# Performance work log

Measured on AMD Instinct MI355X. Metric: run time of the kernel, lower is better.

Reference implementation:

```python
import jax, jax.numpy as jnp
import numpy as np
import math

SAMPLE_RATIO = 0.25
K = 5
EPS = 1e-6

def _cells(loc_orig, H, W):
    # map normalized [-1,1] coords to nearest grid cell index, as in tcformer token2map/map2token
    loc = jnp.clip(loc_orig, -1.0, 1.0)
    px = jnp.clip(jnp.round(0.5 * (loc[..., 0] + 1.0) * W - 0.5).astype(jnp.int32), 0, W - 1)
    py = jnp.clip(jnp.round(0.5 * (loc[..., 1] + 1.0) * H - 0.5).astype(jnp.int32), 0, H - 1)
    return py * W + px  # [B, N0]

def token2map(x, loc_orig, idx_agg, H, W):
    B, N, C = x.shape
    N0 = loc_orig.shape[1]
    cell = _cells(loc_orig, H, W)
    seg = (cell + jnp.arange(B)[:, None] * (H * W)).reshape(-1)
    feat = x[jnp.arange(B)[:, None], idx_agg]  # [B, N0, C] token feature per original point
    sums = jax.ops.segment_sum(feat.reshape(-1, C), seg, num_segments=B * H * W)
    cnt = jax.ops.segment_sum(jnp.ones((B * N0,), x.dtype), seg, num_segments=B * H * W)
    x_map = sums / (cnt[:, None] + EPS)  # per-cell mean over points hitting the cell
    return x_map.reshape(B, H, W, C).transpose(0, 3, 1, 2)

def map2token(x_map, N, loc_orig, idx_agg, agg_weight):
    B, C, H, W = x_map.shape
    cell = _cells(loc_orig, H, W)
    val = x_map.reshape(B, C, H * W).transpose(0, 2, 1)  # [B, HW, C]
    vpt = val[jnp.arange(B)[:, None], cell]              # [B, N0, C] map value at each point
    seg = (idx_agg + jnp.arange(B)[:, None] * N).reshape(-1)
    w = agg_weight.reshape(-1)
    wsum = jax.ops.segment_sum(w, seg, num_segments=B * N) + EPS
    ssum = jax.ops.segment_sum(vpt.reshape(-1, C) * w[:, None], seg, num_segments=B * N)
    return (ssum / wsum[:, None]).reshape(B, N, C)  # agg_weight-weighted mean per token

def token_cluster_merge(x, Ns, idx_agg, weight, k):
    B, N, C = x.shape
    # DPC-KNN clustering (index computation; mirrors torch.no_grad block)
    sq = jnp.sum(x * x, -1)
    d2 = jnp.clip(sq[:, :, None] + sq[:, None, :] - 2.0 * jnp.einsum('bnc,bmc->bnm', x, x), 0.0, None)
    dist = jnp.sqrt(d2) / (C ** 0.5)
    dnear = -jax.lax.top_k(-dist, k)[0]                  # k smallest distances (incl. self)
    density = jnp.exp(-jnp.mean(dnear * dnear, -1))
    mask = density[:, None, :] > density[:, :, None]
    dmax = jnp.max(dist.reshape(B, -1), -1)[:, None, None]
    parent_dist = jnp.min(jnp.where(mask, dist, dmax), -1)  # dist to nearest higher-density token
    score = parent_dist * density
    index_down = jax.lax.top_k(score, Ns)[1]             # [B, Ns] cluster centers
    idx_cluster = jnp.argmin(dist[jnp.arange(B)[:, None], index_down], axis=1)  # [B, N]
    idx_cluster = idx_cluster.at[jnp.arange(B)[:, None], index_down].set(jnp.arange(Ns)[None, :])
    # weighted merge of tokens into clusters
    seg = (idx_cluster + jnp.arange(B)[:, None] * Ns).reshape(-1)
    w = weight.reshape(-1)
    allw = jax.ops.segment_sum(w, seg, num_segments=B * Ns) + EPS
    norm_w = (w / allw[seg]).reshape(B, N)
    x_merged = jax.ops.segment_sum((x * norm_w[:, :, None]).reshape(-1, C), seg, num_segments=B * Ns).reshape(B, Ns, C)
    idx_agg_down = idx_cluster[jnp.arange(B)[:, None], idx_agg]      # compose index maps
    weight_t = norm_w[jnp.arange(B)[:, None], idx_agg][..., None]    # [B, N0, 1]
    return x_merged, idx_agg_down, weight_t

def _forward(x, loc_orig, idx_agg, agg_weight, idx_k_loc, H, W, conv_w, conv_b, skip_w, ln_g, ln_b, conf_w, conf_b):
    B, N, C = x.shape
    x_map = token2map(x, loc_orig, idx_agg, H, W)
    x_map = jax.lax.conv_general_dilated(x_map, conv_w, (2, 2), ((1, 1), (1, 1))) + conv_b[None, :, None, None]
    x_tok = map2token(x_map, N, loc_orig, idx_agg, agg_weight) + jnp.einsum('bnc,oc->bno', x, skip_w)
    mu = jnp.mean(x_tok, -1, keepdims=True)
    var = jnp.mean((x_tok - mu) ** 2, -1, keepdims=True)
    x_tok = (x_tok - mu) / jnp.sqrt(var + 1e-5) * ln_g + ln_b
    conf = jnp.einsum('bnc,oc->bno', x_tok, conf_w) + conf_b
    weight = jnp.exp(conf)
    Ns = max(math.ceil(N * SAMPLE_RATIO), 1)
    x_down, idx_agg_down, weight_t = token_cluster_merge(x_tok, Ns, idx_agg, weight, K)
    agg_weight_down = agg_weight * weight_t
    agg_weight_down = agg_weight_down / jnp.max(agg_weight_down, axis=1, keepdims=True)
    # down_block is an injected submodule; treated as identity passthrough here
    return x_down, idx_agg_down, agg_weight_down

def setup_inputs():
    key = jax.random.key(0)
    ks = jax.random.split(key, 8)
    B, N, C, N0, Cout = 8, 256, 256, 16384, 512
    return {
        'x': jax.random.normal(ks[0], (B, N, C), jnp.float32),
        'loc_orig': jax.random.uniform(ks[1], (B, N0, 2), jnp.float32, -1.0, 1.0),
        'idx_agg': jax.random.randint(ks[2], (B, N0), 0, N),
        'agg_weight': jax.random.uniform(ks[3], (B, N0, 1), jnp.float32, 0.1, 1.0),
        'idx_k_loc': jax.random.randint(ks[4], (B, N0, K), 0, N0),
        'H': 64, 'W': 64,
        'conv_w': jax.random.normal(ks[5], (Cout, C, 3, 3), jnp.float32) * 0.02,
        'conv_b': jnp.zeros((Cout,), jnp.float32),
        'skip_w': jax.random.normal(ks[6], (Cout, C), jnp.float32) * 0.02,
        'ln_g': jnp.ones((Cout,), jnp.float32),
        'ln_b': jnp.zeros((Cout,), jnp.float32),
        'conf_w': jax.random.normal(ks[7], (1, Cout), jnp.float32) * 0.02,
        'conf_b': jnp.zeros((1,), jnp.float32),
    }

def reference(x, loc_orig, idx_agg, agg_weight, idx_k_loc, H, W, conv_w, conv_b, skip_w, ln_g, ln_b, conf_w, conf_b):
    return _forward(x, loc_orig, idx_agg, agg_weight, idx_k_loc, H, W, conv_w, conv_b, skip_w, ln_g, ln_b, conf_w, conf_b)
```

## Files before the change

kernel.cpp:

```cpp
#include <hip/hip_runtime.h>
#include <math.h>

typedef unsigned long long ull;
typedef __attribute__((ext_vector_type(8))) short short8v;
typedef __attribute__((ext_vector_type(4))) float float4v;

#define NB   8
#define NTOK 256
#define CIN  256
#define NP   16384
#define NCO  512
#define HW64 4096
#define OHW  1024
#define NS   64
#define EPS  1e-6f
#define KC   2304
#define NKC  72

constexpr size_t OFF_SUMS = 0;
constexpr size_t OFF_CNT  = OFF_SUMS + (size_t)NB*HW64*CIN;
constexpr size_t OFF_AMAT = OFF_CNT  + (size_t)NB*HW64;
constexpr size_t OFF_ALLW = OFF_AMAT + (size_t)NB*NTOK*OHW;
constexpr size_t OFF_DMAX = OFF_ALLW + (size_t)NB*NS;
constexpr size_t OFF_MAXW = OFF_DMAX + NB;
constexpr size_t ZERO_END = OFF_MAXW + NB;
constexpr size_t OFF_WT   = ZERO_END;
constexpr size_t OFF_SKWT = OFF_WT   + (size_t)KC*NCO;
constexpr size_t OFF_Y    = OFF_SKWT + (size_t)CIN*NCO;
constexpr size_t OFF_C2   = OFF_Y    + (size_t)NB*OHW*NCO;
constexpr size_t OFF_WSUM = OFF_C2   + (size_t)NB*NTOK*NCO;
constexpr size_t OFF_XSKIP= OFF_WSUM + (size_t)NB*NTOK;
constexpr size_t OFF_XTOK = OFF_XSKIP+ (size_t)NB*NTOK*NCO;
constexpr size_t OFF_XPK  = OFF_XTOK + (size_t)NB*NTOK*NCO;
constexpr size_t OFF_WEXP = OFF_XPK  + (size_t)NB*NTOK*NCO;
constexpr size_t OFF_SQ   = OFF_WEXP + (size_t)NB*NTOK;
constexpr size_t OFF_DIST = OFF_SQ   + (size_t)NB*NTOK;
constexpr size_t OFF_DENS = OFF_DIST + (size_t)NB*NTOK*NTOK;
constexpr size_t OFF_SCORE= OFF_DENS + (size_t)NB*NTOK;
constexpr size_t OFF_IND  = OFF_SCORE+ (size_t)NB*NTOK;
constexpr size_t OFF_IDXCL= OFF_IND  + (size_t)NB*NS;
constexpr size_t OFF_NORMW= OFF_IDXCL+ (size_t)NB*NTOK;
constexpr size_t OFF_AWBUF= OFF_NORMW+ (size_t)NB*NTOK;
constexpr size_t OFF_XTPK = OFF_AWBUF+ (size_t)NB*NP;
constexpr size_t OFF_AMATP = OFF_SUMS;
constexpr size_t OFF_XTOKPK= OFF_Y;

__device__ __forceinline__ unsigned pack_hl(float x) {
    unsigned u = __float_as_uint(x);
    unsigned t = u + 0x7fffu + ((u >> 16) & 1u);
    unsigned hibits = t & 0xffff0000u;
    float lo = x - __uint_as_float(hibits);
    unsigned ul = __float_as_uint(lo);
    unsigned lt = ul + 0x7fffu + ((ul >> 16) & 1u);
    return hibits | (lt >> 16);
}
__device__ __forceinline__ unsigned hp2(unsigned w0, unsigned w1) {
    return __builtin_amdgcn_perm(w1, w0, 0x07060302u);
}
__device__ __forceinline__ unsigned lp2(unsigned w0, unsigned w1) {
    return __builtin_amdgcn_perm(w1, w0, 0x05040100u);
}

__global__ void hist(const float* __restrict__ loc, const int* __restrict__ idxagg,
                     const float* __restrict__ aggw,
                     int* __restrict__ cntmat, float* __restrict__ cnt,
                     float* __restrict__ amat) {
    int bp = blockIdx.x*256 + threadIdx.x;
    int b  = bp >> 14;
    float lx = loc[2*bp+0], ly = loc[2*bp+1];
    lx = fminf(fmaxf(lx, -1.f), 1.f);
    ly = fminf(fmaxf(ly, -1.f), 1.f);
    int px = (int)rintf((lx + 1.f)*32.f - 0.5f); px = min(max(px,0),63);
    int py = (int)rintf((ly + 1.f)*32.f - 0.5f); py = min(max(py,0),63);
    int cell = py*64 + px;
    int tok = idxagg[bp];
    atomicAdd(&cntmat[((size_t)(b*HW64 + cell))*NTOK + tok], 1);
    atomicAdd(&cnt[b*HW64 + cell], 1.0f);
    int qx = (int)rintf((lx + 1.f)*16.f - 0.5f); qx = min(max(qx,0),31);
    int qy = (int)rintf((ly + 1.f)*16.f - 0.5f); qy = min(max(qy,0),31);
    atomicAdd(&amat[((size_t)(b*NTOK + tok))*OHW + qy*32 + qx], aggw[bp]);
}

__global__ void cnt_pack(unsigned* __restrict__ m) {
    size_t i = (size_t)blockIdx.x*256 + threadIdx.x;
    int4 v = ((const int4*)m)[i];
    uint4 o;
    o.x = pack_hl((float)v.x); o.y = pack_hl((float)v.y);
    o.z = pack_hl((float)v.z); o.w = pack_hl((float)v.w);
    ((uint4*)m)[i] = o;
}

__global__ void xt_pack(const float* __restrict__ x, unsigned* __restrict__ xtpk) {
    int id = blockIdx.x*256 + threadIdx.x;
    int tok = id & 255, cin = (id >> 8) & 255, b = id >> 16;
    xtpk[id] = pack_hl(x[((size_t)(b*NTOK + tok))*CIN + cin]);
}

__global__ void wtrans(const float* __restrict__ convw, uint4* __restrict__ wtf) {
    int tid = blockIdx.x*256 + threadIdx.x;
    int lane = tid & 63;
    int r1 = tid >> 6;
    int h = r1 & 1;
    int r2 = r1 >> 1;
    int f = r2 & 3;
    int r3 = r2 >> 2;
    int kc = r3 % NKC, mt = r3 / NKC;
    int cout = mt*64 + f*16 + (lane & 15);
    int kb = kc*32 + (lane >> 4)*8;
    unsigned s[8];
    #pragma unroll
    for (int j = 0; j < 8; ++j) {
        int k = kb + j;
        int grp = k >> 8, cin = k & 255;
        unsigned w = pack_hl(convw[(size_t)cout*KC + cin*9 + grp]);
        s[j] = h ? (w & 0xffffu) : (w >> 16);
    }
    uint4 o;
    o.x = s[0] | (s[1]<<16); o.y = s[2] | (s[3]<<16);
    o.z = s[4] | (s[5]<<16); o.w = s[6] | (s[7]<<16);
    wtf[tid] = o;
}

__global__ void pack4(const float4* __restrict__ src, uint4* __restrict__ dst) {
    size_t i = (size_t)blockIdx.x*256 + threadIdx.x;
    float4 v = src[i];
    uint4 o;
    o.x = pack_hl(v.x); o.y = pack_hl(v.y); o.z = pack_hl(v.z); o.w = pack_hl(v.w);
    dst[i] = o;
}

__launch_bounds__(256)
__global__ void conv_gemm(const unsigned* __restrict__ xmap, const uint4* __restrict__ wtf,
                          const float* __restrict__ convb, unsigned* __restrict__ ytp) {
    __shared__ __align__(16) unsigned short Ahi[2][4096], Alo[2][4096];
    int n0 = blockIdx.x * 128;
    int mt = blockIdx.y;
    int m0 = mt * 64;
    int t = threadIdx.x;
    int lane = t & 63, wid = t >> 6;
    int wm = wid >> 1, wn = wid & 1;
    int l15 = lane & 15, l4 = lane >> 4;

    int rowL = t & 127, kg = t >> 7;
    int posG = n0 + rowL;
    int bb = posG >> 10, rem = posG & 1023;
    int oy = rem >> 5, ox = rem & 31;

    int wbA0 = (rowL>>4)*512 + kg*128 + (rowL&15)*8;
    int wbA1 = wbA0 + 256;

    float4v acc[4][2] = {};
    uint4 a00,a01,a10,a11;

    auto loadA = [&](int kc) {
        int grp = kc >> 3;
        int ky = grp/3, kx = grp - 3*ky;
        int iy = 2*oy - 1 + ky, ix = 2*ox - 1 + kx;
        if ((unsigned)iy < 64u && (unsigned)ix < 64u) {
            const unsigned* ap = xmap + ((((size_t)bb*64 + iy)*64 + ix)*256 + (kc&7)*32 + kg*8);
            a00 = *(const uint4*)ap;       a01 = *(const uint4*)(ap + 4);
            a10 = *(const uint4*)(ap + 16); a11 = *(const uint4*)(ap + 20);
        } else {
            a00 = make_uint4(0,0,0,0); a01 = a00; a10 = a00; a11 = a00;
        }
    };
    auto repackA = [&](int buf) {
        uint4 h, l;
        h.x=hp2(a00.x,a00.y); h.y=hp2(a00.z,a00.w); h.z=hp2(a01.x,a01.y); h.w=hp2(a01.z,a01.w);
        l.x=lp2(a00.x,a00.y); l.y=lp2(a00.z,a00.w); l.z=lp2(a01.x,a01.y); l.w=lp2(a01.z,a01.w);
        *(uint4*)&Ahi[buf][wbA0] = h; *(uint4*)&Alo[buf][wbA0] = l;
        h.x=hp2(a10.x,a10.y); h.y=hp2(a10.z,a10.w); h.z=hp2(a11.x,a11.y); h.w=hp2(a11.z,a11.w);
        l.x=lp2(a10.x,a10.y); l.y=lp2(a10.z,a10.w); l.z=lp2(a11.x,a11.y); l.w=lp2(a11.z,a11.w);
        *(uint4*)&Ahi[buf][wbA1] = h; *(uint4*)&Alo[buf][wbA1] = l;
    };
    const uint4* wbase = wtf + ((size_t)(((mt*NKC)*4 + wn*2)*2))*64 + lane;

    short8v bhc[2], blc[2], bhn[2], bln[2];
    #pragma unroll
    for (int q = 0; q < 2; ++q) {
        bhc[q] = *(const short8v*)(wbase + q*128);
        blc[q] = *(const short8v*)(wbase + q*128 + 64);
    }
    loadA(0);
    repackA(0);
    __syncthreads();
    int cur = 0;

    for (int kc = 0; kc < NKC; ++kc) {
        bool notlast = (kc + 1 < NKC);
        if (notlast) {
            loadA(kc+1);
            const uint4* wb = wbase + (size_t)(kc+1)*512;
            #pragma unroll
            for (int q = 0; q < 2; ++q) {
                bhn[q] = *(const short8v*)(wb + q*128);
                bln[q] = *(const short8v*)(wb + q*128 + 64);
            }
        }
        #pragma unroll
        for (int p = 0; p < 4; ++p) {
            int off = (wm*4 + p)*512 + l4*128 + l15*8;
            short8v ah = *(const short8v*)&Ahi[cur][off];
            short8v al = *(const short8v*)&Alo[cur][off];
            #pragma unroll
            for (int q = 0; q < 2; ++q) {
                acc[p][q] = __builtin_amdgcn_mfma_f32_16x16x32_bf16(ah, bhc[q], acc[p][q], 0, 0, 0);
                acc[p][q] = __builtin_amdgcn_mfma_f32_16x16x32_bf16(ah, blc[q], acc[p][q], 0, 0, 0);
                acc[p][q] = __builtin_amdgcn_mfma_f32_16x16x32_bf16(al, bhc[q], acc[p][q], 0, 0, 0);
            }
        }
        if (notlast) {
            repackA(cur ^ 1);
            #pragma unroll
            for (int q = 0; q < 2; ++q) { bhc[q] = bhn[q]; blc[q] = bln[q]; }
        }
        __syncthreads();
        cur ^= 1;
    }

    int bbk = n0 >> 10;
    int pos0 = (n0 & 1023) + wm*64;
    #pragma unroll
    for (int p = 0; p < 4; ++p) {
        int posb = pos0 + p*16 + l4*4;
        #pragma unroll
        for (int q = 0; q < 2; ++q) {
            int col = m0 + wn*32 + q*16 + l15;
            float bv = convb[col];
            uint4 o;
            o.x = pack_hl(acc[p][q][0] + bv);
            o.y = pack_hl(acc[p][q][1] + bv);
            o.z = pack_hl(acc[p][q][2] + bv);
            o.w = pack_hl(acc[p][q][3] + bv);
            *(uint4*)&ytp[((size_t)(bbk*NCO + col))*OHW + posb] = o;
        }
    }
}

template<int MODE, int TM, int TN>
__launch_bounds__(256)
__global__ void gemm_pk(const unsigned* __restrict__ A, const unsigned* __restrict__ B,
                        float* __restrict__ C, int K, int N,
                        long sA, long sB, long sC,
                        const float* __restrict__ aux, unsigned* __restrict__ dmaxU) {
    constexpr int NA = TM/64, NBs = TN/64;
    constexpr int WSM = TM/64;
    constexpr int WSN = 4/WSM;
    constexpr int TWM = TM/WSM, TWN = TN/WSN;
    constexpr int P = TWM/16, Q = TWN/16;
    __shared__ __align__(16) unsigned short Ahi[TM*32], Alo[TM*32];
    __shared__ __align__(16) unsigned short Bhi[TN*32], Blo[TN*32];
    int z = blockIdx.z;
    const unsigned* Ab = A + (size_t)z*sA;
    const unsigned* Bb = B + (size_t)z*sB;
    float* Cb = C + (size_t)z*sC;
    int n0 = blockIdx.x*TN, m0 = blockIdx.y*TM;
    int t = threadIdx.x;
    int lane = t & 63, wid = t >> 6;
    int wm = (WSM==2) ? (wid >> 1) : 0;
    int wn = (WSM==2) ? (wid & 1)  : wid;
    int l15 = lane & 15, l4 = lane >> 4;

    int rowA = t & (TM-1), kgA = t / TM;
    int rowB = t & (TN-1), kgB = t / TN;
    const unsigned* arow = Ab + (size_t)(m0 + rowA)*K + kgA*8;
    const unsigned* brw  = Bb + (size_t)(n0 + rowB)*K + kgB*8;
    int wbA = (rowA>>4)*512 + kgA*128 + (rowA&15)*8;
    int wbB = (rowB>>4)*512 + kgB*128 + (rowB&15)*8;

    float4v acc[P][Q] = {};
    uint4 ra[NA][2], rb[NBs][2];
    auto loadA = [&](int kc) {
        #pragma unroll
        for (int s = 0; s < NA; ++s) {
            const unsigned* p = arow + (size_t)kc*32 + s*16;
            ra[s][0] = *(const uint4*)p; ra[s][1] = *(const uint4*)(p + 4);
        }
    };
    auto loadB = [&](int kc) {
        #pragma unroll
        for (int s = 0; s < NBs; ++s) {
            const unsigned* p = brw + (size_t)kc*32 + s*16;
            rb[s][0] = *(const uint4*)p; rb[s][1] = *(const uint4*)(p + 4);
        }
    };
    loadA(0); loadB(0);
    int nkc = K >> 5;

    for (int kc = 0; kc < nkc; ++kc) {
        __syncthreads();
        uint4 h, l;
        #pragma unroll
        for (int s = 0; s < NA; ++s) {
            uint4 u0 = ra[s][0], u1 = ra[s][1];
            h.x=hp2(u0.x,u0.y); h.y=hp2(u0.z,u0.w); h.z=hp2(u1.x,u1.y); h.w=hp2(u1.z,u1.w);
            l.x=lp2(u0.x,u0.y); l.y=lp2(u0.z,u0.w); l.z=lp2(u1.x,u1.y); l.w=lp2(u1.z,u1.w);
            *(uint4*)&Ahi[wbA + s*256] = h; *(uint4*)&Alo[wbA + s*256] = l;
        }
        #pragma unroll
        for (int s = 0; s < NBs; ++s) {
            uint4 u0 = rb[s][0], u1 = rb[s][1];
            h.x=hp2(u0.x,u0.y); h.y=hp2(u0.z,u0.w); h.z=hp2(u1.x,u1.y); h.w=hp2(u1.z,u1.w);
            l.x=lp2(u0.x,u0.y); l.y=lp2(u0.z,u0.w); l.z=lp2(u1.x,u1.y); l.w=lp2(u1.z,u1.w);
            *(uint4*)&Bhi[wbB + s*256] = h; *(uint4*)&Blo[wbB + s*256] = l;
        }
        __syncthreads();
        if (kc + 1 < nkc) { loadA(kc+1); loadB(kc+1); }

        short8v bh[Q], bl[Q];
        #pragma unroll
        for (int q = 0; q < Q; ++q) {
            int off = (wn*Q + q)*512 + l4*128 + l15*8;
            bh[q] = *(const short8v*)&Bhi[off];
            bl[q] = *(const short8v*)&Blo[off];
        }
        #pragma unroll
        for (int p = 0; p < P; ++p) {
            int off = (wm*P + p)*512 + l4*128 + l15*8;
            short8v ah = *(const short8v*)&Ahi[off];
            short8v al = *(const short8v*)&Alo[off];
            #pragma unroll
            for (int q = 0; q < Q; ++q) {
                acc[p][q] = __builtin_amdgcn_mfma_f32_16x16x32_bf16(ah, bh[q], acc[p][q], 0, 0, 0);
                acc[p][q] = __builtin_amdgcn_mfma_f32_16x16x32_bf16(ah, bl[q], acc[p][q], 0, 0, 0);
                acc[p][q] = __builtin_amdgcn_mfma_f32_16x16x32_bf16(al, bh[q], acc[p][q], 0, 0, 0);
            }
        }
    }

    if (MODE == 0) {
        #pragma unroll
        for (int p = 0; p < P; ++p) {
            int mb = m0 + wm*TWM + p*16 + l4*4;
            #pragma unroll
            for (int q = 0; q < Q; ++q) {
                int n = n0 + wn*TWN + q*16 + l15;
                #pragma unroll
                for (int r = 0; r < 4; ++r)
                    Cb[(size_t)(mb + r)*N + n] = acc[p][q][r];
            }
        }
    } else if (MODE == 1) {
        const float inv = 1.0f / sqrtf(512.0f);
        const float* sqb = aux + (size_t)z*NTOK;
        float tmax = 0.f;
        #pragma unroll
        for (int p = 0; p < P; ++p) {
            int mb = m0 + wm*TWM + p*16 + l4*4;
            #pragma unroll
            for (int q = 0; q < Q; ++q) {
                int n = n0 + wn*TWN + q*16 + l15;
                float sn = sqb[n];
                #pragma unroll
                for (int r = 0; r < 4; ++r) {
                    float d2 = sqb[mb + r] + sn - 2.0f*acc[p][q][r];
                    float d = sqrtf(fmaxf(d2, 0.0f)) * inv;
                    Cb[(size_t)(mb + r)*N + n] = d;
                    tmax = fmaxf(tmax, d);
                }
            }
        }
        __shared__ float redm[4];
        #pragma unroll
        for (int off = 32; off; off >>= 1) tmax = fmaxf(tmax, __shfl_xor(tmax, off, 64));
        if (lane == 0) redm[wid] = tmax;
        __syncthreads();
        if (t == 0) {
            float m = fmaxf(fmaxf(redm[0], redm[1]), fmaxf(redm[2], redm[3]));
            atomicMax(dmaxU + z, __float_as_uint(m));
        }
    } else {
        unsigned* Cu = (unsigned*)Cb;
        const float* cntb = aux + (size_t)z*HW64;
        #pragma unroll
        for (int p = 0; p < P; ++p) {
            int mb = m0 + wm*TWM + p*16 + l4*4;
            #pragma unroll
            for (int q = 0; q < Q; ++q) {
                int n = n0 + wn*TWN + q*16 + l15;
                #pragma unroll
                for (int r = 0; r < 4; ++r) {
                    float v = acc[p][q][r] / (cntb[mb + r] + EPS);
                    Cu[(size_t)(mb + r)*N + n] = pack_hl(v);
                }
            }
        }
    }
}

__global__ void wsum_rows(const float* __restrict__ amat, float* __restrict__ wsum) {
    int row = blockIdx.x*4 + (threadIdx.x >> 6);
    int lane = threadIdx.x & 63;
    const float* ar = amat + (size_t)row*OHW;
    float s = 0.f;
    #pragma unroll
    for (int r = 0; r < 16; ++r) s += ar[lane + 64*r];
    #pragma unroll
    for (int off = 32; off; off >>= 1) s += __shfl_xor(s, off, 64);
    if (lane == 0) wsum[row] = s;
}

__device__ __forceinline__ float block_sum256(float v, float* red) {
    #pragma unroll
    for (int off = 32; off; off >>= 1) v += __shfl_xor(v, off, 64);
    __syncthreads();
    if ((threadIdx.x & 63) == 0) red[threadIdx.x >> 6] = v;
    __syncthreads();
    return red[0] + red[1] + red[2] + red[3];
}

__global__ void ln_conf(const float* __restrict__ C2, const float* __restrict__ wsum,
                        const float* __restrict__ xskip, const float* __restrict__ g,
                        const float* __restrict__ be, const float* __restrict__ confw,
                        const float* __restrict__ confb, float* __restrict__ xtok,
                        unsigned* __restrict__ xtokpk,
                        float* __restrict__ wexp, float* __restrict__ sqv) {
    __shared__ float red[4];
    int row = blockIdx.x, t = threadIdx.x;
    float ws = wsum[row] + EPS;
    size_t base = (size_t)row*NCO;
    float v0 = C2[base + t]       / ws + xskip[base + t];
    float v1 = C2[base + t + 256] / ws + xskip[base + t + 256];
    float mu  = block_sum256(v0 + v1, red) / 512.0f;
    float d0 = v0 - mu, d1 = v1 - mu;
    float var = block_sum256(d0*d0 + d1*d1, red) / 512.0f;
    float sv = sqrtf(var + 1e-5f);
    float x0 = d0/sv * g[t]       + be[t];
    float x1 = d1/sv * g[t + 256] + be[t + 256];
    xtok[base + t] = x0;
    xtok[base + t + 256] = x1;
    xtokpk[base + t] = pack_hl(x0);
    xtokpk[base + t + 256] = pack_hl(x1);
    float cs = block_sum256(x0*confw[t] + x1*confw[t + 256], red);
    float qs = block_sum256(x0*x0 + x1*x1, red);
    if (t == 0) {
        wexp[row] = expf(cs + confb[0]);
        sqv[row]  = qs;
    }
}

__global__ void knn_dens(const float* __restrict__ dist, float* __restrict__ dens) {
    int row = blockIdx.x*4 + (threadIdx.x >> 6);
    int lane = threadIdx.x & 63;
    const float* dr = dist + (size_t)row*NTOK;
    float v0 = dr[lane], v1 = dr[lane+64], v2 = dr[lane+128], v3 = dr[lane+192];
    float acc = 0.f;
    #pragma unroll
    for (int it = 0; it < 5; ++it) {
        float lm = fminf(fminf(v0, v1), fminf(v2, v3));
        float gm = lm;
        #pragma unroll
        for (int off = 32; off; off >>= 1) gm = fminf(gm, __shfl_xor(gm, off, 64));
        acc += gm*gm;
        ull ball = __ballot(lm == gm);
        int first = __ffsll(ball) - 1;
        if (lane == first) {
            if      (v0 == gm) v0 = 1e30f;
            else if (v1 == gm) v1 = 1e30f;
            else if (v2 == gm) v2 = 1e30f;
            else               v3 = 1e30f;
        }
    }
    if (lane == 0) dens[row] = expf(-(acc/5.0f));
}

__global__ void parent_score(const float* __restrict__ dist, const float* __restrict__ dens,
                             const unsigned* __restrict__ dmaxU, float* __restrict__ score) {
    int row = blockIdx.x*4 + (threadIdx.x >> 6);
    int lane = threadIdx.x & 63;
    int b = row >> 8;
    float di = dens[row];
    float dm = __uint_as_float(dmaxU[b]);
    const float* dr = dist + (size_t)row*NTOK;
    const float* db = dens + (size_t)b*NTOK;
    float pd = dm;
    #pragma unroll
    for (int r = 0; r < 4; ++r) {
        int j = lane + 64*r;
        pd = fminf(pd, (db[j] > di) ? dr[j] : dm);
    }
    #pragma unroll
    for (int off = 32; off; off >>= 1) pd = fminf(pd, __shfl_xor(pd, off, 64));
    if (lane == 0) score[row] = pd * di;
}

__global__ void topk64(const float* __restrict__ score, int* __restrict__ ind) {
    int b = blockIdx.x, lane = threadIdx.x;
    const float* sb = score + b*NTOK;
    ull k0, k1, k2, k3;
    {
        unsigned i0 = lane, i1 = lane+64, i2 = lane+128, i3 = lane+192;
        k0 = ((ull)(__float_as_uint(sb[i0]) + 1u) << 32) | (unsigned)(4095 - i0);
        k1 = ((ull)(__float_as_uint(sb[i1]) + 1u) << 32) | (unsigned)(4095 - i1);
        k2 = ((ull)(__float_as_uint(sb[i2]) + 1u) << 32) | (unsigned)(4095 - i2);
        k3 = ((ull)(__float_as_uint(sb[i3]) + 1u) << 32) | (unsigned)(4095 - i3);
    }
    for (int it = 0; it < 64; ++it) {
        ull lm = k0;
        if (k1 > lm) lm = k1;
        if (k2 > lm) lm = k2;
        if (k3 > lm) lm = k3;
        ull gm = lm;
        #pragma unroll
        for (int off = 32; off; off >>= 1) {
            ull o = __shfl_xor(gm, off, 64);
            if (o > gm) gm = o;
        }
        if (lane == 0) ind[b*NS + it] = 4095 - (int)(gm & 0xffffffffull);
        if      (k0 == gm) k0 = 0;
        else if (k1 == gm) k1 = 0;
        else if (k2 == gm) k2 = 0;
        else if (k3 == gm) k3 = 0;
    }
}

__global__ void assign_k(const float* __restrict__ dist, const int* __restrict__ ind,
                         int* __restrict__ idxcl) {
    int row = blockIdx.x*4 + (threadIdx.x >> 6);
    int lane = threadIdx.x & 63;
    int b = row >> 8, i = row & 255;
    int center = ind[b*NS + lane];
    float d = dist[((size_t)(b*NTOK + center))*NTOK + i];
    ull key = ((ull)__float_as_uint(d) << 32) | (unsigned)lane;
    #pragma unroll
    for (int off = 32; off; off >>= 1) {
        ull o = __shfl_xor(key, off, 64);
        if (o < key) key = o;
    }
    if (lane == 0) idxcl[row] = (int)(key & 0xffffffffull);
}

__global__ void center_set(const int* __restrict__ ind, int* __restrict__ idxcl) {
    int id = threadIdx.x;
    int b = id >> 6, s = id & 63;
    idxcl[b*NTOK + ind[id]] = s;
}

__global__ void allw_acc(const int* __restrict__ idxcl, const float* __restrict__ wexp,
                         float* __restrict__ allw) {
    int b = blockIdx.x, i = threadIdx.x;
    atomicAdd(&allw[b*NS + idxcl[b*NTOK + i]], wexp[b*NTOK + i]);
}

__global__ void normw_k(const int* __restrict__ idxcl, const float* __restrict__ wexp,
                        const float* __restrict__ allw, float* __restrict__ normw) {
    int b = blockIdx.x, i = threadIdx.x;
    normw[b*NTOK + i] = wexp[b*NTOK + i] / (allw[b*NS + idxcl[b*NTOK + i]] + EPS);
}

__global__ void merge_k(const float* __restrict__ xtok, const int* __restrict__ idxcl,
                        const float* __restrict__ normw, float* __restrict__ xout) {
    int row = blockIdx.x, t = threadIdx.x;
    int b = row >> 8;
    int cl = idxcl[row];
    float nw = normw[row];
    float* o = xout + ((size_t)(b*NS + cl))*NCO;
    const float* xr = xtok + (size_t)row*NCO;
    atomicAdd(&o[t],       xr[t]       * nw);
    atomicAdd(&o[t + 256], xr[t + 256] * nw);
}

__global__ void out_idx_aw(const int* __restrict__ idxagg, const float* __restrict__ aggw,
                           const int* __restrict__ idxcl, const float* __restrict__ normw,
                           float* __restrict__ dout, float* __restrict__ awbuf,
                           unsigned* __restrict__ maxw) {
    __shared__ float red[4];
    int bp = blockIdx.x*256 + threadIdx.x;
    int b = bp >> 14;
    int tok = idxagg[bp];
    int cl = idxcl[b*NTOK + tok];
    dout[(size_t)NB*NS*NCO + bp] = (float)cl;
    float aw = aggw[bp] * normw[b*NTOK + tok];
    awbuf[bp] = aw;
    float m = aw;
    #pragma unroll
    for (int off = 32; off; off >>= 1) m = fmaxf(m, __shfl_xor(m, off, 64));
    if ((threadIdx.x & 63) == 0) red[threadIdx.x >> 6] = m;
    __syncthreads();
    if (threadIdx.x == 0) {
        float mm = fmaxf(fmaxf(red[0], red[1]), fmaxf(red[2], red[3]));
        atomicMax(&maxw[b], __float_as_uint(mm));
    }
}

__global__ void aw_final(const float* __restrict__ awbuf, const float* __restrict__ maxw,
                         float* __restrict__ dout) {
    int bp = blockIdx.x*256 + threadIdx.x;
    int b = bp >> 14;
    dout[(size_t)NB*NS*NCO + (size_t)NB*NP + bp] = awbuf[bp] / maxw[b];
}

extern "C" void kernel_launch(void* const* d_in, const int* in_sizes, int n_in,
                              void* d_out, int out_size, void* d_ws, size_t ws_size,
                              hipStream_t stream) {
    const float* x      = (const float*)d_in[0];
    const float* loc    = (const float*)d_in[1];
    const int*   idxagg = (const int*)  d_in[2];
    const float* aggw   = (const float*)d_in[3];
    const float* convw  = (const float*)d_in[7];
    const float* convb  = (const float*)d_in[8];
    const float* skipw  = (const float*)d_in[9];
    const float* lng    = (const float*)d_in[10];
    const float* lnb    = (const float*)d_in[11];
    const float* confw  = (const float*)d_in[12];
    const float* confb  = (const float*)d_in[13];

    float* ws = (float*)d_ws;
    float* dout = (float*)d_out;

    (void)hipMemsetAsync(ws, 0, ZERO_END*sizeof(float), stream);
    (void)hipMemsetAsync(dout, 0, (size_t)NB*NS*NCO*sizeof(float), stream);

    hist<<<dim3(NB*NP/256), 256, 0, stream>>>(loc, idxagg, aggw,
                                              (int*)(ws + OFF_SUMS), ws + OFF_CNT, ws + OFF_AMAT);
    cnt_pack<<<dim3(NB*HW64*CIN/1024), 256, 0, stream>>>((unsigned*)(ws + OFF_SUMS));
    xt_pack<<<dim3(NB*CIN*NTOK/256), 256, 0, stream>>>(x, (unsigned*)(ws + OFF_XTPK));
    wtrans<<<dim3(1152), 256, 0, stream>>>(convw, (uint4*)(ws + OFF_WT));
    pack4<<<dim3(CIN*NCO/1024), 256, 0, stream>>>((const float4*)skipw, (uint4*)(ws + OFF_SKWT));
    pack4<<<dim3(NB*NTOK*CIN/1024), 256, 0, stream>>>((const float4*)x, (uint4*)(ws + OFF_XPK));

    gemm_pk<2,128,128><<<dim3(2, 32, 8), 256, 0, stream>>>((const unsigned*)(ws + OFF_SUMS),
                                                   (const unsigned*)(ws + OFF_XTPK),
                                                   ws + OFF_SUMS, NTOK, CIN,
                                                   (long)HW64*NTOK, (long)CIN*NTOK, (long)HW64*CIN,
                                                   ws + OFF_CNT, nullptr);

    conv_gemm<<<dim3(64, 8), 256, 0, stream>>>((const unsigned*)(ws + OFF_SUMS),
                                               (const uint4*)(ws + OFF_WT), convb,
                                               (unsigned*)(ws + OFF_Y));

    wsum_rows<<<dim3(NB*NTOK/4), 256, 0, stream>>>(ws + OFF_AMAT, ws + OFF_WSUM);
    pack4<<<dim3(NB*NTOK*OHW/1024), 256, 0, stream>>>((const float4*)(ws + OFF_AMAT),
                                                      (uint4*)(ws + OFF_AMATP));
    gemm_pk<0,64,64><<<dim3(8, 4, 8), 256, 0, stream>>>((const unsigned*)(ws + OFF_AMATP),
                                                  (const unsigned*)(ws + OFF_Y),
                                                  ws + OFF_C2, OHW, NCO,
                                                  (long)NTOK*OHW, (long)NCO*OHW, (long)NTOK*NCO,
                                                  nullptr, nullptr);
    gemm_pk<0,64,64><<<dim3(8, 32, 1), 256, 0, stream>>>((const unsigned*)(ws + OFF_XPK),
                                                   (const unsigned*)(ws + OFF_SKWT),
                                                   ws + OFF_XSKIP, CIN, NCO, 0, 0, 0,
                                                   nullptr, nullptr);

    ln_conf<<<dim3(NB*NTOK), 256, 0, stream>>>(ws + OFF_C2, ws + OFF_WSUM, ws + OFF_XSKIP,
                                               lng, lnb, confw, confb,
                                               ws + OFF_XTOK, (unsigned*)(ws + OFF_XTOKPK),
                                               ws + OFF_WEXP, ws + OFF_SQ);

    gemm_pk<1,64,64><<<dim3(4, 4, 8), 256, 0, stream>>>((const unsigned*)(ws + OFF_XTOKPK),
                                                  (const unsigned*)(ws + OFF_XTOKPK),
                                                  ws + OFF_DIST, NCO, NTOK,
                                                  (long)NTOK*NCO, (long)NTOK*NCO, (long)NTOK*NTOK,
                                                  ws + OFF_SQ, (unsigned*)(ws + OFF_DMAX));

    knn_dens<<<dim3(NB*NTOK/4), 256, 0, stream>>>(ws + OFF_DIST, ws + OFF_DENS);
    parent_score<<<dim3(NB*NTOK/4), 256, 0, stream>>>(ws + OFF_DIST, ws + OFF_DENS,
                                                      (const unsigned*)(ws + OFF_DMAX), ws + OFF_SCORE);
    topk64<<<dim3(NB), 64, 0, stream>>>(ws + OFF_SCORE, (int*)(ws + OFF_IND));
    assign_k<<<dim3(NB*NTOK/4), 256, 0, stream>>>(ws + OFF_DIST, (const int*)(ws + OFF_IND),
                                                  (int*)(ws + OFF_IDXCL));
    center_set<<<dim3(1), 512, 0, stream>>>((const int*)(ws + OFF_IND), (int*)(ws + OFF_IDXCL));
    allw_acc<<<dim3(NB), 256, 0, stream>>>((const int*)(ws + OFF_IDXCL), ws + OFF_WEXP, ws + OFF_ALLW);
    normw_k<<<dim3(NB), 256, 0, stream>>>((const int*)(ws + OFF_IDXCL), ws + OFF_WEXP,
                                          ws + OFF_ALLW, ws + OFF_NORMW);
    merge_k<<<dim3(NB*NTOK), 256, 0, stream>>>(ws + OFF_XTOK, (const int*)(ws + OFF_IDXCL),
                                               ws + OFF_NORMW, dout);
    out_idx_aw<<<dim3(NB*NP/256), 256, 0, stream>>>(idxagg, aggw, (const int*)(ws + OFF_IDXCL),
                                                    ws + OFF_NORMW, dout, ws + OFF_AWBUF,
                                                    (unsigned*)(ws + OFF_MAXW));
    aw_final<<<dim3(NB*NP/256), 256, 0, stream>>>(ws + OFF_AWBUF, (const float*)(ws + OFF_MAXW), dout);
}
```

Before: 304.3 us.

## Store token map as split bf16 hi/lo planes and stage conv A via global_load_lds

The token-to-map GEMM now lives in its own kernel. It writes the normalized map as separate hi and lo bf16 planes in a 128-row tiled layout, replacing packed hi/lo words. The conv GEMM then copies A tiles straight from global into LDS with global_load_lds. Out-of-bounds taps point at a zeroed guard buffer, which removes the register staging and permute repack in the main loop. The packed amat buffer moves to a new offset so it no longer aliases the planes, at the cost of strided 16-bit stores in the map epilogue.

```diff
diff --git a/kernel.cpp b/kernel.cpp
--- a/kernel.cpp
+++ b/kernel.cpp
@@ -17,13 +17,20 @@
 #define KC   2304
 #define NKC  72
 
+#define AS1 __attribute__((address_space(1)))
+#define AS3 __attribute__((address_space(3)))
+__device__ __forceinline__ void gl_lds16(const unsigned short* g, unsigned short* l) {
+    __builtin_amdgcn_global_load_lds((const AS1 unsigned*)g, (AS3 unsigned*)l, 16, 0, 0);
+}
+
 constexpr size_t OFF_SUMS = 0;
 constexpr size_t OFF_CNT  = OFF_SUMS + (size_t)NB*HW64*CIN;
 constexpr size_t OFF_AMAT = OFF_CNT  + (size_t)NB*HW64;
 constexpr size_t OFF_ALLW = OFF_AMAT + (size_t)NB*NTOK*OHW;
 constexpr size_t OFF_DMAX = OFF_ALLW + (size_t)NB*NS;
 constexpr size_t OFF_MAXW = OFF_DMAX + NB;
-constexpr size_t ZERO_END = OFF_MAXW + NB;
+constexpr size_t OFF_ZG   = OFF_MAXW + NB;
+constexpr size_t ZERO_END = OFF_ZG + 8;
 constexpr size_t OFF_WT   = ZERO_END;
 constexpr size_t OFF_SKWT = OFF_WT   + (size_t)KC*NCO;
 constexpr size_t OFF_Y    = OFF_SKWT + (size_t)CIN*NCO;
@@ -42,7 +49,7 @@
 constexpr size_t OFF_NORMW= OFF_IDXCL+ (size_t)NB*NTOK;
 constexpr size_t OFF_AWBUF= OFF_NORMW+ (size_t)NB*NTOK;
 constexpr size_t OFF_XTPK = OFF_AWBUF+ (size_t)NB*NP;
-constexpr size_t OFF_AMATP = OFF_SUMS;
+constexpr size_t OFF_AMATP2= OFF_XTPK + (size_t)NB*CIN*NTOK;
 constexpr size_t OFF_XTOKPK= OFF_Y;
 
 __device__ __forceinline__ unsigned pack_hl(float x) {
@@ -129,67 +136,150 @@
     dst[i] = o;
 }
 
+__launch_bounds__(512)
+__global__ void map_gemm(const unsigned* __restrict__ A, const unsigned* __restrict__ B,
+                         const float* __restrict__ cnt, unsigned short* __restrict__ planes) {
+    __shared__ __align__(16) unsigned short Ah[4096];
+    __shared__ __align__(16) unsigned short Bh[8192], Bl[8192];
+    int z = blockIdx.z, m0 = blockIdx.y*128;
+    const unsigned* Ab = A + ((size_t)z*HW64 + m0)*NTOK;
+    const unsigned* Bb = B + (size_t)z*CIN*NTOK;
+    int t = threadIdx.x, lane = t & 63;
+    int w = t >> 6;
+    int wm = w >> 2, wn = w & 3;
+    int l15 = lane & 15, l4 = lane >> 4;
+    int rowA = t & 127, kgA = t >> 7;
+    int rowB = t & 255, kgB0 = (t >> 8)*2;
+    const unsigned* arow = Ab + (size_t)rowA*NTOK + kgA*8;
+    const unsigned* brow = Bb + (size_t)rowB*NTOK + kgB0*8;
+    int wbA = (rowA>>4)*512 + kgA*128 + (rowA&15)*8;
+    int wbB = (rowB>>4)*512 + kgB0*128 + (rowB&15)*8;
+
+    float4v acc[4][4] = {};
+    uint4 ra0, ra1, rb[2][2];
+    auto loadA = [&](int kc) {
+        const unsigned* p = arow + kc*32;
+        ra0 = *(const uint4*)p; ra1 = *(const uint4*)(p + 4);
+    };
+    auto loadB = [&](int kc) {
+        #pragma unroll
+        for (int s = 0; s < 2; ++s) {
+            const unsigned* p = brow + kc*32 + s*8;
+            rb[s][0] = *(const uint4*)p; rb[s][1] = *(const uint4*)(p + 4);
+        }
+    };
+    loadA(0); loadB(0);
+
+    for (int kc = 0; kc < 8; ++kc) {
+        __syncthreads();
+        uint4 h, l;
+        h.x=hp2(ra0.x,ra0.y); h.y=hp2(ra0.z,ra0.w); h.z=hp2(ra1.x,ra1.y); h.w=hp2(ra1.z,ra1.w);
+        *(uint4*)&Ah[wbA] = h;
+        #pragma unroll
+        for (int s = 0; s < 2; ++s) {
+            uint4 u0 = rb[s][0], u1 = rb[s][1];
+            h.x=hp2(u0.x,u0.y); h.y=hp2(u0.z,u0.w); h.z=hp2(u1.x,u1.y); h.w=hp2(u1.z,u1.w);
+            l.x=lp2(u0.x,u0.y); l.y=lp2(u0.z,u0.w); l.z=lp2(u1.x,u1.y); l.w=lp2(u1.z,u1.w);
+            *(uint4*)&Bh[wbB + s*128] = h; *(uint4*)&Bl[wbB + s*128] = l;
+        }
+        __syncthreads();
+        if (kc < 7) { loadA(kc+1); loadB(kc+1); }
+
+        short8v bh[4], bl[4];
+        #pragma unroll
+        for (int q = 0; q < 4; ++q) {
+            int off = (wn*4 + q)*512 + l4*128 + l15*8;
+            bh[q] = *(const short8v*)&Bh[off];
+            bl[q] = *(const short8v*)&Bl[off];
+        }
+        #pragma unroll
+        for (int p = 0; p < 4; ++p) {
+            int off = (wm*4 + p)*512 + l4*128 + l15*8;
+            short8v ah = *(const short8v*)&Ah[off];
+            #pragma unroll
+            for (int q = 0; q < 4; ++q) {
+                acc[p][q] = __builtin_amdgcn_mfma_f32_16x16x32_bf16(ah, bh[q], acc[p][q], 0, 0, 0);
+                acc[p][q] = __builtin_amdgcn_mfma_f32_16x16x32_bf16(ah, bl[q], acc[p][q], 0, 0, 0);
+            }
+        }
+    }
+
+    const float* cntb = cnt + (size_t)z*HW64;
+    #pragma unroll
+    for (int p = 0; p < 4; ++p) {
+        int mb = m0 + wm*64 + p*16 + l4*4;
+        #pragma unroll
+        for (int q = 0; q < 4; ++q) {
+            int n = wn*64 + q*16 + l15;
+            #pragma unroll
+            for (int r = 0; r < 4; ++r) {
+                float v = acc[p][q][r] / (cntb[mb + r] + EPS);
+                unsigned pk = pack_hl(v);
+                size_t grow = (size_t)z*HW64 + mb + r;
+                size_t base = (grow >> 7)*65536 + (grow & 127)*256 + n;
+                planes[base]         = (unsigned short)(pk >> 16);
+                planes[base + 32768] = (unsigned short)(pk & 0xffffu);
+            }
+        }
+    }
+}
+
 __launch_bounds__(256)
-__global__ void conv_gemm(const unsigned* __restrict__ xmap, const uint4* __restrict__ wtf,
-                          const float* __restrict__ convb, unsigned* __restrict__ ytp) {
-    __shared__ __align__(16) unsigned short Ahi[2][4096], Alo[2][4096];
+__global__ void conv_gemm(const unsigned short* __restrict__ planes,
+                          const uint4* __restrict__ wtf,
+                          const float* __restrict__ convb,
+                          const unsigned short* __restrict__ zg,
+                          unsigned* __restrict__ ytp) {
+    __shared__ __align__(16) unsigned short AH[2][4096], AL[2][4096];
     int n0 = blockIdx.x * 128;
     int mt = blockIdx.y;
     int m0 = mt * 64;
     int t = threadIdx.x;
-    int lane = t & 63, wid = t >> 6;
-    int wm = wid >> 1, wn = wid & 1;
+    int lane = t & 63, w = t >> 6;
+    int wm = w >> 1, wn = w & 1;
     int l15 = lane & 15, l4 = lane >> 4;
-
-    int rowL = t & 127, kg = t >> 7;
-    int posG = n0 + rowL;
-    int bb = posG >> 10, rem = posG & 1023;
-    int oy = rem >> 5, ox = rem & 31;
-
-    int wbA0 = (rowL>>4)*512 + kg*128 + (rowL&15)*8;
-    int wbA1 = wbA0 + 256;
-
-    float4v acc[4][2] = {};
-    uint4 a00,a01,a10,a11;
-
-    auto loadA = [&](int kc) {
+    int kg = l4;
+
+    int bbS[2], oyS[2], oxS[2];
+    #pragma unroll
+    for (int s = 0; s < 2; ++s) {
+        int pos = n0 + (w + s*4)*16 + l15;
+        bbS[s] = pos >> 10; int rem = pos & 1023;
+        oyS[s] = rem >> 5; oxS[s] = rem & 31;
+    }
+    auto stage = [&](int kc, int buf) {
         int grp = kc >> 3;
         int ky = grp/3, kx = grp - 3*ky;
-        int iy = 2*oy - 1 + ky, ix = 2*ox - 1 + kx;
-        if ((unsigned)iy < 64u && (unsigned)ix < 64u) {
-            const unsigned* ap = xmap + ((((size_t)bb*64 + iy)*64 + ix)*256 + (kc&7)*32 + kg*8);
-            a00 = *(const uint4*)ap;       a01 = *(const uint4*)(ap + 4);
-            a10 = *(const uint4*)(ap + 16); a11 = *(const uint4*)(ap + 20);
-        } else {
-            a00 = make_uint4(0,0,0,0); a01 = a00; a10 = a00; a11 = a00;
+        int kin = (kc & 7)*32 + kg*8;
+        #pragma unroll
+        for (int s = 0; s < 2; ++s) {
+            int iy = 2*oyS[s] - 1 + ky, ix = 2*oxS[s] - 1 + kx;
+            bool ok = ((unsigned)iy < 64u) && ((unsigned)ix < 64u);
+            int srow = bbS[s]*HW64 + iy*64 + ix;
+            const unsigned short* sp = planes + ((size_t)(srow >> 7))*65536 + (srow & 127)*256 + kin;
+            const unsigned short* ph = ok ? sp : zg;
+            const unsigned short* pl = ok ? sp + 32768 : zg;
+            gl_lds16(ph, &AH[buf][(w + s*4)*512]);
+            gl_lds16(pl, &AL[buf][(w + s*4)*512]);
         }
     };
-    auto repackA = [&](int buf) {
-        uint4 h, l;
-        h.x=hp2(a00.x,a00.y); h.y=hp2(a00.z,a00.w); h.z=hp2(a01.x,a01.y); h.w=hp2(a01.z,a01.w);
-        l.x=lp2(a00.x,a00.y); l.y=lp2(a00.z,a00.w); l.z=lp2(a01.x,a01.y); l.w=lp2(a01.z,a01.w);
-        *(uint4*)&Ahi[buf][wbA0] = h; *(uint4*)&Alo[buf][wbA0] = l;
-        h.x=hp2(a10.x,a10.y); h.y=hp2(a10.z,a10.w); h.z=hp2(a11.x,a11.y); h.w=hp2(a11.z,a11.w);
-        l.x=lp2(a10.x,a10.y); l.y=lp2(a10.z,a10.w); l.z=lp2(a11.x,a11.y); l.w=lp2(a11.z,a11.w);
-        *(uint4*)&Ahi[buf][wbA1] = h; *(uint4*)&Alo[buf][wbA1] = l;
-    };
+
     const uint4* wbase = wtf + ((size_t)(((mt*NKC)*4 + wn*2)*2))*64 + lane;
-
+    float4v acc[4][2] = {};
     short8v bhc[2], blc[2], bhn[2], bln[2];
     #pragma unroll
     for (int q = 0; q < 2; ++q) {
         bhc[q] = *(const short8v*)(wbase + q*128);
         blc[q] = *(const short8v*)(wbase + q*128 + 64);
     }
-    loadA(0);
-    repackA(0);
+    stage(0, 0);
     __syncthreads();
     int cur = 0;
 
     for (int kc = 0; kc < NKC; ++kc) {
-        bool notlast = (kc + 1 < NKC);
-        if (notlast) {
-            loadA(kc+1);
+        bool nl = (kc + 1 < NKC);
+        if (nl) {
+            stage(kc+1, cur ^ 1);
             const uint4* wb = wbase + (size_t)(kc+1)*512;
             #pragma unroll
             for (int q = 0; q < 2; ++q) {
@@ -200,8 +290,8 @@
         #pragma unroll
         for (int p = 0; p < 4; ++p) {
             int off = (wm*4 + p)*512 + l4*128 + l15*8;
-            short8v ah = *(const short8v*)&Ahi[cur][off];
-            short8v al = *(const short8v*)&Alo[cur][off];
+            short8v ah = *(const short8v*)&AH[cur][off];
+            short8v al = *(const short8v*)&AL[cur][off];
             #pragma unroll
             for (int q = 0; q < 2; ++q) {
                 acc[p][q] = __builtin_amdgcn_mfma_f32_16x16x32_bf16(ah, bhc[q], acc[p][q], 0, 0, 0);
@@ -209,8 +299,7 @@
                 acc[p][q] = __builtin_amdgcn_mfma_f32_16x16x32_bf16(al, bhc[q], acc[p][q], 0, 0, 0);
             }
         }
-        if (notlast) {
-            repackA(cur ^ 1);
+        if (nl) {
             #pragma unroll
             for (int q = 0; q < 2; ++q) { bhc[q] = bhn[q]; blc[q] = bln[q]; }
         }
@@ -340,7 +429,7 @@
                     Cb[(size_t)(mb + r)*N + n] = acc[p][q][r];
             }
         }
-    } else if (MODE == 1) {
+    } else {
         const float inv = 1.0f / sqrtf(512.0f);
         const float* sqb = aux + (size_t)z*NTOK;
         float tmax = 0.f;
@@ -368,22 +457,6 @@
         if (t == 0) {
             float m = fmaxf(fmaxf(redm[0], redm[1]), fmaxf(redm[2], redm[3]));
             atomicMax(dmaxU + z, __float_as_uint(m));
-        }
-    } else {
-        unsigned* Cu = (unsigned*)Cb;
-        const float* cntb = aux + (size_t)z*HW64;
-        #pragma unroll
-        for (int p = 0; p < P; ++p) {
-            int mb = m0 + wm*TWM + p*16 + l4*4;
-            #pragma unroll
-            for (int q = 0; q < Q; ++q) {
-                int n = n0 + wn*TWN + q*16 + l15;
-                #pragma unroll
-                for (int r = 0; r < 4; ++r) {
-                    float v = acc[p][q][r] / (cntb[mb + r] + EPS);
-                    Cu[(size_t)(mb + r)*N + n] = pack_hl(v);
-                }
-            }
         }
     }
 }
@@ -619,20 +692,20 @@
     pack4<<<dim3(CIN*NCO/1024), 256, 0, stream>>>((const float4*)skipw, (uint4*)(ws + OFF_SKWT));
     pack4<<<dim3(NB*NTOK*CIN/1024), 256, 0, stream>>>((const float4*)x, (uint4*)(ws + OFF_XPK));
 
-    gemm_pk<2,128,128><<<dim3(2, 32, 8), 256, 0, stream>>>((const unsigned*)(ws + OFF_SUMS),
-                                                   (const unsigned*)(ws + OFF_XTPK),
-                                                   ws + OFF_SUMS, NTOK, CIN,
-                                                   (long)HW64*NTOK, (long)CIN*NTOK, (long)HW64*CIN,
-                                                   ws + OFF_CNT, nullptr);
-
-    conv_gemm<<<dim3(64, 8), 256, 0, stream>>>((const unsigned*)(ws + OFF_SUMS),
+    map_gemm<<<dim3(1, 32, 8), 512, 0, stream>>>((const unsigned*)(ws + OFF_SUMS),
+                                                 (const unsigned*)(ws + OFF_XTPK),
+                                                 ws + OFF_CNT,
+                                                 (unsigned short*)(ws + OFF_SUMS));
+
+    conv_gemm<<<dim3(64, 8), 256, 0, stream>>>((const unsigned short*)(ws + OFF_SUMS),
                                                (const uint4*)(ws + OFF_WT), convb,
+                                               (const unsigned short*)(ws + OFF_ZG),
                                                (unsigned*)(ws + OFF_Y));
 
     wsum_rows<<<dim3(NB*NTOK/4), 256, 0, stream>>>(ws + OFF_AMAT, ws + OFF_WSUM);
     pack4<<<dim3(NB*NTOK*OHW/1024), 256, 0, stream>>>((const float4*)(ws + OFF_AMAT),
-                                                      (uint4*)(ws + OFF_AMATP));
-    gemm_pk<0,64,64><<<dim3(8, 4, 8), 256, 0, stream>>>((const unsigned*)(ws + OFF_AMATP),
+                                                      (uint4*)(ws + OFF_AMATP2));
+    gemm_pk<0,64,64><<<dim3(8, 4, 8), 256, 0, stream>>>((const unsigned*)(ws + OFF_AMATP2),
                                                   (const unsigned*)(ws + OFF_Y),
                                                   ws + OFF_C2, OHW, NCO,
                                                   (long)NTOK*OHW, (long)NCO*OHW, (long)NTOK*NCO,
```

Measured after the change: 317.5 us. 1.04x slower.
